# Kernel tuning notes

Measured on AMD Instinct MI355X. Metric: run time of the kernel, lower is better.

The kernel has to match this reference:

```python
import jax, jax.numpy as jnp
import numpy as np

D_MODEL = 1024
N_HEADS = 16
D_FF = 4 * D_MODEL
CTX = 2048
EPS = 1e-5


def setup_inputs() -> dict:
    key = jax.random.key(0)
    ks = jax.random.split(key, 8)
    s = 0.02
    z = jax.random.normal(ks[0], (2, CTX, D_MODEL), dtype=jnp.float32)
    W_Q = jax.random.normal(ks[1], (D_MODEL, D_MODEL), dtype=jnp.float32) * s
    W_K = jax.random.normal(ks[2], (D_MODEL, D_MODEL), dtype=jnp.float32) * s
    W_V = jax.random.normal(ks[3], (D_MODEL, D_MODEL), dtype=jnp.float32) * s
    W_O = jax.random.normal(ks[4], (D_MODEL, D_MODEL), dtype=jnp.float32) * s
    W_fc = jax.random.normal(ks[5], (D_MODEL, D_FF), dtype=jnp.float32) * s
    W_proj = jax.random.normal(ks[6], (D_FF, D_MODEL), dtype=jnp.float32) * s
    g1 = jnp.ones((D_MODEL,), dtype=jnp.float32)
    g2 = jnp.ones((D_MODEL,), dtype=jnp.float32)
    return {"z": z, "W_Q": W_Q, "W_K": W_K, "W_V": W_V, "W_O": W_O,
            "W_fc": W_fc, "W_proj": W_proj, "g1": g1, "g2": g2}


def rmsnorm(x, gain):
    rms = jnp.sqrt(jnp.sum(x * x, axis=-1, keepdims=True) / x.shape[-1] + EPS)
    return (x / rms) * gain


def gelu_erf(x):
    return x * 0.5 * (1.0 + jax.lax.erf(x / jnp.sqrt(2.0).astype(x.dtype)))


def attention(zn, W_Q, W_K, W_V, W_O):
    B, T, D = zn.shape
    H = N_HEADS
    dh = D // H
    # [B,T,D] -> [B,H,T,dh]
    def split(x):
        return x.reshape(B, T, H, dh).transpose(0, 2, 1, 3)
    Q = split(zn @ W_Q)
    K = split(zn @ W_K)
    V = split(zn @ W_V)
    scores = jnp.einsum('bhtd,bhsd->bhts', Q, K) / jnp.sqrt(jnp.float32(dh))
    causal = jnp.triu(jnp.ones((T, T), dtype=bool), k=1)  # True above diagonal -> masked
    scores = jnp.where(causal[None, None], -jnp.inf, scores)
    weights = jax.nn.softmax(scores, axis=-1)
    ctx = jnp.einsum('bhts,bhsd->bhtd', weights, V)
    ctx = ctx.transpose(0, 2, 1, 3).reshape(B, T, D)
    return ctx @ W_O


def reference(z, W_Q, W_K, W_V, W_O, W_fc, W_proj, g1, g2):
    # pre-norm GPT block: z + attn(norm1(z)); then + ffn(norm2(z))
    z = z + attention(rmsnorm(z, g1), W_Q, W_K, W_V, W_O)
    h = rmsnorm(z, g2)
    ffn = gelu_erf(h @ W_fc) @ W_proj
    return z + ffn
```

## Files before the change

### kernel.cpp

```cpp
#include <hip/hip_runtime.h>
#include <hip/hip_bf16.h>
#include <math.h>


typedef __bf16 bf16x8 __attribute__((ext_vector_type(8)));
typedef float  f32x4  __attribute__((ext_vector_type(4)));

#define MFMA_16x16x32_BF16(A, B, C) __builtin_amdgcn_mfma_f32_16x16x32_bf16((A), (B), (C), 0, 0, 0)

#define GLDS16(g, l) __builtin_amdgcn_global_load_lds( \
    (const __attribute__((address_space(1))) void*)(g), \
    (__attribute__((address_space(3))) void*)(l), 16, 0, 0)

__global__ __launch_bounds__(256) void transconv_all_kernel(
    const float* __restrict__ W_Q, const float* __restrict__ W_K,
    const float* __restrict__ W_V, const float* __restrict__ W_O,
    const float* __restrict__ W_fc, const float* __restrict__ W_proj,
    __bf16* __restrict__ WtQKV, __bf16* __restrict__ WtO,
    __bf16* __restrict__ Wtfc, __bf16* __restrict__ Wtproj)
{
    const int id = blockIdx.x;
    const float* src;
    __bf16* dst;
    int K, N, nx, t;
    if (id < 4096) {
        const int wsel = id >> 10;
        t = id & 1023;
        src = (wsel == 0) ? W_Q : (wsel == 1) ? W_K : (wsel == 2) ? W_V : W_O;
        dst = (wsel < 3) ? (WtQKV + (size_t)wsel * 1048576) : WtO;
        K = 1024; N = 1024; nx = 32;
    } else if (id < 8192) {
        t = id - 4096; src = W_fc; dst = Wtfc; K = 1024; N = 4096; nx = 128;
    } else {
        t = id - 8192; src = W_proj; dst = Wtproj; K = 4096; N = 1024; nx = 32;
    }
    const int n0 = (t % nx) * 32, k0 = (t / nx) * 32;

    __shared__ float tile[32][33];
    const int c = threadIdx.x & 31, r = threadIdx.x >> 5;
#pragma unroll
    for (int i = 0; i < 4; ++i)
        tile[r + 8 * i][c] = src[(size_t)(k0 + r + 8 * i) * N + n0 + c];
    __syncthreads();
#pragma unroll
    for (int i = 0; i < 4; ++i)
        dst[(size_t)(n0 + r + 8 * i) * K + k0 + c] = (__bf16)tile[c][r + 8 * i];
}

__global__ __launch_bounds__(256) void rmsnorm_kernel(
    const float* __restrict__ x, const float* __restrict__ gain,
    __bf16* __restrict__ out)
{
    const int row = blockIdx.x, t = threadIdx.x;
    const float4 v = ((const float4*)(x + (size_t)row * 1024))[t];
    float ss = v.x * v.x + v.y * v.y + v.z * v.z + v.w * v.w;
#pragma unroll
    for (int m = 1; m < 64; m <<= 1) ss += __shfl_xor(ss, m);
    __shared__ float red[4];
    const int wid = t >> 6, lane = t & 63;
    if (lane == 0) red[wid] = ss;
    __syncthreads();
    const float tot = red[0] + red[1] + red[2] + red[3];
    const float inv = rsqrtf(tot * (1.0f / 1024.0f) + 1e-5f);
    const float4 gv = ((const float4*)gain)[t];
    __bf16* o = out + (size_t)row * 1024 + t * 4;
    o[0] = (__bf16)(v.x * inv * gv.x);
    o[1] = (__bf16)(v.y * inv * gv.y);
    o[2] = (__bf16)(v.z * inv * gv.z);
    o[3] = (__bf16)(v.w * inv * gv.w);
}

template <int EPI>
__device__ __forceinline__ void epi_write(
    void* outp, const float* res, int N, int rowg, int colg, float v)
{
    if constexpr (EPI == 1) {
        const size_t idx = (size_t)rowg * N + colg;
        ((float*)outp)[idx] = res[idx] + v;
    } else if constexpr (EPI == 2) {
        const size_t idx = (size_t)rowg * N + colg;
        ((__bf16*)outp)[idx] =
            (__bf16)(0.5f * v * (1.0f + erff(v * 0.70710678118654752f)));
    } else if constexpr (EPI == 3) {
        const size_t idx = (size_t)rowg * N + colg;
        ((float*)outp)[idx] += v;
    } else {
        __bf16* base = (__bf16*)outp;
        const int seg = colg >> 10;
        const int cg = colg & 1023;
        if (seg < 2) {
            base[(size_t)seg * 4194304 + (size_t)rowg * 1024 + cg] = (__bf16)v;
        } else {
            const int tt = rowg & 2047;
            const int r32 = tt & 31;
            const int p = ((r32 & 12) << 1) | ((r32 >> 2) & 4) | (r32 & 3);
            base[8388608 +
                 ((size_t)((rowg >> 11) * 16 + (cg >> 6)) * 64 + (cg & 63)) * 2048 +
                 ((tt & ~31) | p)] = (__bf16)v;
        }
    }
}

template <int EPI>
__global__ __launch_bounds__(512, 2) void gemm256(
    const __bf16* __restrict__ A, const __bf16* __restrict__ Bt,
    void* __restrict__ outp, const float* __restrict__ res,
    int M, int N, int K)
{
    __shared__ __bf16 As[2][2][128 * 64];
    __shared__ __bf16 Bs[2][2][128 * 64];
    const int tid = threadIdx.x;

    const int gx = gridDim.x, nwg = gx * gridDim.y;
    int bid = blockIdx.y * gx + blockIdx.x;
    if ((nwg & 7) == 0) bid = (bid & 7) * (nwg >> 3) + (bid >> 3);
    const int m0 = (bid / gx) * 256, n0 = (bid % gx) * 256;

    const int lane = tid & 63, w = tid >> 6;
    const int wr = w >> 2, wc = w & 3;
    const int lr = lane & 15, g = lane >> 4;
    const int srow8 = lane >> 3, schunk = (lane & 7) ^ srow8;
    const int xk = lr & 7;
    const int wch = wc >> 1, bro = (wc & 1) * 64;

    const __bf16* Ab = A + (size_t)m0 * K;
    const __bf16* Bb = Bt + (size_t)n0 * K;

    auto STG = [&](const __bf16* gb, __bf16* lds, int kt, int half) {
        const __bf16* src = gb + (size_t)(half * 128) * K + (kt << 6);
#pragma unroll
        for (int j = 0; j < 2; ++j) {
            const int sidx = j * 8 + w;
            GLDS16(src + (size_t)(sidx * 8 + srow8) * K + schunk * 8, lds + sidx * 512);
        }
    };

    f32x4 acc[8][4] = {};
    bf16x8 af[2][4], bf[2][4];

#define LAF(BUF, QM) do {                                                       \
    _Pragma("unroll") for (int i_ = 0; i_ < 4; ++i_)                            \
    _Pragma("unroll") for (int kk_ = 0; kk_ < 2; ++kk_)                         \
        af[kk_][i_] = *(const bf16x8*)&As[BUF][wr]                              \
            [((QM) * 64 + i_ * 16 + lr) * 64 + (((kk_ * 4 + g) ^ xk) << 3)];    \
    } while (0)

#define LBF(BUF, QN) do {                                                       \
    _Pragma("unroll") for (int i_ = 0; i_ < 2; ++i_)                            \
    _Pragma("unroll") for (int kk_ = 0; kk_ < 2; ++kk_)                         \
        bf[kk_][(QN) * 2 + i_] = *(const bf16x8*)&Bs[BUF][wch]                  \
            [(bro + ((QN) * 2 + i_) * 16 + lr) * 64 + (((kk_ * 4 + g) ^ xk) << 3)]; \
    } while (0)

#define MMQ(QM, QN) do {                                                        \
    __builtin_amdgcn_s_setprio(1);                                              \
    _Pragma("unroll") for (int kk_ = 0; kk_ < 2; ++kk_)                         \
    _Pragma("unroll") for (int i_ = 0; i_ < 4; ++i_)                            \
    _Pragma("unroll") for (int n_ = 0; n_ < 2; ++n_)                            \
        acc[(QM) * 4 + i_][(QN) * 2 + n_] = MFMA_16x16x32_BF16(                 \
            af[kk_][i_], bf[kk_][(QN) * 2 + n_], acc[(QM) * 4 + i_][(QN) * 2 + n_]); \
    __builtin_amdgcn_s_setprio(0);                                              \
    } while (0)

#define BAR()  __builtin_amdgcn_s_barrier()
#define VMC(N_) asm volatile("s_waitcnt vmcnt(" #N_ ")" ::: "memory")
#define SGB0() __builtin_amdgcn_sched_barrier(0)

    const int nt = K >> 6, niter = nt >> 1;

    STG(Ab, &As[0][0][0], 0, 0); STG(Ab, &As[0][1][0], 0, 1);
    STG(Bb, &Bs[0][0][0], 0, 0); STG(Bb, &Bs[0][1][0], 0, 1);
    STG(Bb, &Bs[1][0][0], 1, 0); STG(Bb, &Bs[1][1][0], 1, 1);

    for (int i = 0; i < niter - 1; ++i) {
        const int t1 = 2 * i + 1;
        STG(Ab, &As[1][0][0], t1, 0);
        VMC(6); BAR(); SGB0();
        LAF(0, 0); LBF(0, 0); MMQ(0, 0); BAR();
        LBF(0, 1); STG(Ab, &As[1][1][0], t1, 1); BAR(); MMQ(0, 1); BAR();
        LAF(0, 1); STG(Bb, &Bs[0][0][0], t1 + 1, 0); BAR(); MMQ(1, 0); BAR();
        STG(Bb, &Bs[0][1][0], t1 + 1, 1); BAR(); MMQ(1, 1); BAR();
        STG(Ab, &As[0][0][0], t1 + 1, 0);
        VMC(6); BAR(); SGB0();
        LAF(1, 0); LBF(1, 0); MMQ(0, 0); BAR();
        LBF(1, 1); STG(Ab, &As[0][1][0], t1 + 1, 1); BAR(); MMQ(0, 1); BAR();
        LAF(1, 1); STG(Bb, &Bs[1][0][0], t1 + 2, 0); BAR(); MMQ(1, 0); BAR();
        STG(Bb, &Bs[1][1][0], t1 + 2, 1); BAR(); MMQ(1, 1); BAR();
    }
    {
        STG(Ab, &As[1][0][0], nt - 1, 0);
        VMC(6); BAR(); SGB0();
        LAF(0, 0); LBF(0, 0); MMQ(0, 0); BAR();
        LBF(0, 1); STG(Ab, &As[1][1][0], nt - 1, 1); BAR(); MMQ(0, 1); BAR();
        LAF(0, 1); BAR(); MMQ(1, 0); BAR();
        BAR(); MMQ(1, 1); BAR();
        VMC(0); BAR(); SGB0();
        LAF(1, 0); LBF(1, 0); MMQ(0, 0); BAR();
        LBF(1, 1); BAR(); MMQ(0, 1); BAR();
        LAF(1, 1); BAR(); MMQ(1, 0); BAR();
        BAR(); MMQ(1, 1); BAR();
    }
#undef LAF
#undef LBF
#undef MMQ
#undef BAR
#undef VMC
#undef SGB0

#pragma unroll
    for (int mi = 0; mi < 8; ++mi)
#pragma unroll
        for (int ni = 0; ni < 4; ++ni) {
            const int colg = n0 + wc * 64 + ni * 16 + lr;
#pragma unroll
            for (int r = 0; r < 4; ++r) {
                const int rowg = m0 + wr * 128 + mi * 16 + 4 * g + r;
                epi_write<EPI>(outp, res, N, rowg, colg, acc[mi][ni][r]);
            }
        }
}

template <int BM, int BN, int EPI>
__global__ __launch_bounds__(256) void gemm_bf16(
    const __bf16* __restrict__ A, const __bf16* __restrict__ Bt,
    void* __restrict__ outp, const float* __restrict__ res,
    int M, int N, int K)
{
    __shared__ __bf16 As[2][BM * 64];
    __shared__ __bf16 Bs[2][BN * 64];
    const int tid = threadIdx.x;

    const int gx = gridDim.x, nwg = gx * gridDim.y;
    int bid = blockIdx.y * gx + blockIdx.x;
    if ((nwg & 7) == 0) bid = (bid & 7) * (nwg >> 3) + (bid >> 3);
    const int m0 = (bid / gx) * BM, n0 = (bid % gx) * BN;

    const int lane = tid & 63, w = tid >> 6;
    const int wm = w >> 1, wn = w & 1;
    const int lr = lane & 15, g = lane >> 4;
    const int srow = lane >> 3;
    const int scol = ((lane & 7) ^ srow) * 8;
    const int xr8 = lr & 7;

    constexpr int MI = BM / 32, NI = BN / 32;
    f32x4 acc[MI][NI] = {};

    const __bf16* Abase = A + (size_t)m0 * K;
    const __bf16* Bbase = Bt + (size_t)n0 * K;

    auto STAGE = [&](int kb, int buf) {
#pragma unroll
        for (int j = 0; j < BM / 32; ++j) {
            const int s = j * 4 + w;
            GLDS16(Abase + (size_t)(s * 8 + srow) * K + kb + scol, &As[buf][s * 512]);
        }
#pragma unroll
        for (int j = 0; j < BN / 32; ++j) {
            const int s = j * 4 + w;
            GLDS16(Bbase + (size_t)(s * 8 + srow) * K + kb + scol, &Bs[buf][s * 512]);
        }
    };

    const int nt = K >> 6;
    STAGE(0, 0);
    __syncthreads();

    for (int t = 0; t < nt; ++t) {
        const int cur = t & 1;
        if (t + 1 < nt) STAGE((t + 1) << 6, cur ^ 1);

        bf16x8 af[2][MI], bfr[2][NI];
#pragma unroll
        for (int kk = 0; kk < 2; ++kk) {
#pragma unroll
            for (int i = 0; i < MI; ++i)
                af[kk][i] = *(const bf16x8*)
                    &As[cur][(wm * (BM / 2) + i * 16 + lr) * 64 + (((kk * 4 + g) ^ xr8) << 3)];
#pragma unroll
            for (int i = 0; i < NI; ++i)
                bfr[kk][i] = *(const bf16x8*)
                    &Bs[cur][(wn * (BN / 2) + i * 16 + lr) * 64 + (((kk * 4 + g) ^ xr8) << 3)];
        }
#pragma unroll
        for (int kk = 0; kk < 2; ++kk)
#pragma unroll
            for (int mi = 0; mi < MI; ++mi)
#pragma unroll
                for (int ni = 0; ni < NI; ++ni)
                    acc[mi][ni] = MFMA_16x16x32_BF16(af[kk][mi], bfr[kk][ni], acc[mi][ni]);
        if (t + 1 < nt) __syncthreads();
    }

#pragma unroll
    for (int mi = 0; mi < MI; ++mi)
#pragma unroll
        for (int ni = 0; ni < NI; ++ni) {
            const int colg = n0 + wn * (BN / 2) + ni * 16 + lr;
#pragma unroll
            for (int r = 0; r < 4; ++r) {
                const int rowg = m0 + wm * (BM / 2) + mi * 16 + 4 * g + r;
                epi_write<EPI>(outp, res, N, rowg, colg, acc[mi][ni][r]);
            }
        }
}

__global__ __launch_bounds__(256) void attn_kernel(
    const __bf16* __restrict__ Q, const __bf16* __restrict__ Kb,
    const __bf16* __restrict__ Vt, __bf16* __restrict__ ctx)
{
    const int Dm = 1024, T = 2048;
    const int tid = threadIdx.x;
    const int w = tid >> 6, lane = tid & 63;
    const int lr = lane & 15, g = lane >> 4;
    const int bx = blockIdx.x;
    const int j = bx >> 5, bh = bx & 31, b = bh >> 4, h = bh & 15;
    const int qc = (j < 8) ? j : (j < 16) ? 39 - j : (j < 24) ? j - 8 : 47 - j;
    const int qbase = qc * 64 + w * 16;
    const size_t rowoff = (size_t)b * T;
    const __bf16* Qp = Q + rowoff * Dm + h * 64;
    const __bf16* Kp = Kb + rowoff * Dm + h * 64;
    const __bf16* Vtp = Vt + (size_t)bh * 64 * 2048;

    __shared__ __bf16 Ks[2][64 * 64];
    __shared__ __bf16 Vs[2][64 * 64];

    bf16x8 qf0 = *(const bf16x8*)&Qp[(size_t)(qbase + lr) * Dm + g * 8];
    bf16x8 qf1 = *(const bf16x8*)&Qp[(size_t)(qbase + lr) * Dm + 32 + g * 8];
    const float qsc = 0.125f * 1.44269504088896340736f;
#pragma unroll
    for (int jj = 0; jj < 8; ++jj) {
        qf0[jj] = (__bf16)((float)qf0[jj] * qsc);
        qf1[jj] = (__bf16)((float)qf1[jj] * qsc);
    }

    const int srow = lane >> 3;
    const int schunk = (lane & 7) ^ srow;

    f32x4 acc[4] = {};
    float m_s = -__builtin_inff(), l_s = 0.0f;
    const int nsteps = qc + 1;
    const f32x4 zacc = {0.0f, 0.0f, 0.0f, 0.0f};
    const int xr = (lr & 7) << 3;
    const int qg = qbase + lr;

#pragma unroll
    for (int jj = 0; jj < 2; ++jj) {
        const int row = jj * 32 + w * 8 + srow;
        GLDS16(Kp + (size_t)row * Dm + schunk * 8, &Ks[0][(jj * 32 + w * 8) * 64]);
        GLDS16(Vtp + (size_t)row * T + schunk * 8, &Vs[0][(jj * 32 + w * 8) * 64]);
    }
    __syncthreads();

    for (int t = 0; t < nsteps; ++t) {
        const int kvb = t * 64, cur = t & 1;
        if (t + 1 < nsteps) {
#pragma unroll
            for (int jj = 0; jj < 2; ++jj) {
                const int row = jj * 32 + w * 8 + srow;
                GLDS16(Kp + (size_t)(kvb + 64 + row) * Dm + schunk * 8,
                       &Ks[cur ^ 1][(jj * 32 + w * 8) * 64]);
                GLDS16(Vtp + (size_t)row * T + kvb + 64 + schunk * 8,
                       &Vs[cur ^ 1][(jj * 32 + w * 8) * 64]);
            }
        }

        float sv[4][4];
#pragma unroll
        for (int s4 = 0; s4 < 4; ++s4) {
            const int kv0 = kvb + s4 * 16;
            if (kv0 <= qbase + 15) {
                const int row = s4 * 16 + lr;
                const bf16x8 kfa = *(const bf16x8*)&Ks[cur][row * 64 + ((g * 8) ^ xr)];
                const bf16x8 kfb = *(const bf16x8*)&Ks[cur][row * 64 + ((32 + g * 8) ^ xr)];
                f32x4 st = MFMA_16x16x32_BF16(kfa, qf0, zacc);
                st = MFMA_16x16x32_BF16(kfb, qf1, st);
                const bool domask = (kv0 + 15 > qbase);
#pragma unroll
                for (int r = 0; r < 4; ++r) {
                    float x = st[r];
                    if (domask && (kv0 + 4 * g + r > qg)) x = -__builtin_inff();
                    sv[s4][r] = x;
                }
            } else {
#pragma unroll
                for (int r = 0; r < 4; ++r) sv[s4][r] = -__builtin_inff();
            }
        }

        float tm = sv[0][0];
#pragma unroll
        for (int s4 = 0; s4 < 4; ++s4)
#pragma unroll
            for (int r = 0; r < 4; ++r) tm = fmaxf(tm, sv[s4][r]);
        tm = fmaxf(tm, __shfl_xor(tm, 16));
        tm = fmaxf(tm, __shfl_xor(tm, 32));

        float m_use = m_s;
        if (!__all(tm - m_s <= 11.5f)) {
            m_use = fmaxf(m_s, tm);
            const float corr = exp2f(m_s - m_use);
            l_s *= corr;
            float cr[4];
#pragma unroll
            for (int r = 0; r < 4; ++r) cr[r] = __shfl(corr, 4 * g + r);
#pragma unroll
            for (int ct = 0; ct < 4; ++ct) {
                acc[ct][0] *= cr[0]; acc[ct][1] *= cr[1];
                acc[ct][2] *= cr[2]; acc[ct][3] *= cr[3];
            }
            m_s = m_use;
        }

        float rs = 0.0f;
#pragma unroll
        for (int s4 = 0; s4 < 4; ++s4)
#pragma unroll
            for (int r = 0; r < 4; ++r) {
                sv[s4][r] = exp2f(sv[s4][r] - m_use);
                rs += sv[s4][r];
            }
        rs += __shfl_xor(rs, 16);
        rs += __shfl_xor(rs, 32);
        l_s += rs;

        bf16x8 pa0, pa1;
#pragma unroll
        for (int r = 0; r < 4; ++r) {
            pa0[r] = (__bf16)sv[0][r];
            pa0[4 + r] = (__bf16)sv[1][r];
            pa1[r] = (__bf16)sv[2][r];
            pa1[4 + r] = (__bf16)sv[3][r];
        }
        const bool liveB = (kvb + 32 <= qbase + 15);
#pragma unroll
        for (int ct = 0; ct < 4; ++ct) {
            const __bf16* vrow = &Vs[cur][(ct * 16 + lr) * 64];
            const bf16x8 vf = *(const bf16x8*)&vrow[(8 * g) ^ xr];
            acc[ct] = MFMA_16x16x32_BF16(pa0, vf, acc[ct]);
            if (liveB) {
                const bf16x8 vf2 = *(const bf16x8*)&vrow[(32 + 8 * g) ^ xr];
                acc[ct] = MFMA_16x16x32_BF16(pa1, vf2, acc[ct]);
            }
        }
        __syncthreads();
    }

    const float il = __builtin_amdgcn_rcpf(l_s);
    float dn[4];
#pragma unroll
    for (int r = 0; r < 4; ++r) dn[r] = __shfl(il, 4 * g + r);
#pragma unroll
    for (int ct = 0; ct < 4; ++ct)
#pragma unroll
        for (int r = 0; r < 4; ++r)
            ctx[(rowoff + qbase + 4 * g + r) * Dm + h * 64 + ct * 16 + lr] =
                (__bf16)(acc[ct][r] * dn[r]);
}

extern "C" void kernel_launch(void* const* d_in, const int* in_sizes, int n_in,
                              void* d_out, int out_size, void* d_ws, size_t ws_size,
                              hipStream_t stream)
{
    (void)in_sizes; (void)n_in; (void)out_size; (void)ws_size;
    const float* z      = (const float*)d_in[0];
    const float* W_Q    = (const float*)d_in[1];
    const float* W_K    = (const float*)d_in[2];
    const float* W_V    = (const float*)d_in[3];
    const float* W_O    = (const float*)d_in[4];
    const float* W_fc   = (const float*)d_in[5];
    const float* W_proj = (const float*)d_in[6];
    const float* g1     = (const float*)d_in[7];
    const float* g2     = (const float*)d_in[8];
    float* out = (float*)d_out;

    char* ws = (char*)d_ws;
    const size_t MB = (size_t)1 << 20;
    __bf16* WtQKV  = (__bf16*)(ws + 0 * MB);
    __bf16* WtO    = (__bf16*)(ws + 6 * MB);
    __bf16* Wtfc   = (__bf16*)(ws + 8 * MB);
    __bf16* Wtproj = (__bf16*)(ws + 16 * MB);
    __bf16* zn     = (__bf16*)(ws + 24 * MB);
    __bf16* Qb     = (__bf16*)(ws + 32 * MB);
    __bf16* Kbuf   = (__bf16*)(ws + 40 * MB);
    __bf16* Vtb    = (__bf16*)(ws + 48 * MB);
    __bf16* ffn1   = (__bf16*)(ws + 40 * MB);
    __bf16* ctx    = zn;
    __bf16* hb     = Qb;

    const int Tt = 2048, Dm = 1024, Bb = 2, M = Bb * Tt, DFF = 4096;
    const dim3 blk256(256), blk512(512);

    transconv_all_kernel<<<12288, blk256, 0, stream>>>(
        W_Q, W_K, W_V, W_O, W_fc, W_proj, WtQKV, WtO, Wtfc, Wtproj);

    rmsnorm_kernel<<<M, blk256, 0, stream>>>(z, g1, zn);

    gemm_bf16<128, 64, 4><<<dim3(48, 32), blk256, 0, stream>>>(
        zn, WtQKV, Qb, nullptr, M, 3072, Dm);

    attn_kernel<<<1024, blk256, 0, stream>>>(Qb, Kbuf, Vtb, ctx);

    gemm_bf16<128, 64, 1><<<dim3(16, 32), blk256, 0, stream>>>(
        ctx, WtO, out, z, M, Dm, Dm);

    rmsnorm_kernel<<<M, blk256, 0, stream>>>(out, g2, hb);

    gemm256<2><<<dim3(16, 16), blk512, 0, stream>>>(
        hb, Wtfc, ffn1, nullptr, M, DFF, Dm);

    gemm_bf16<128, 64, 3><<<dim3(16, 32), blk256, 0, stream>>>(
        ffn1, Wtproj, out, nullptr, M, Dm, DFF);
}
```

Measured before the change: 269.9 us.

## Split-K the FFN down-projection with a reduce kernel; enlarge QKV GEMM tile

The FFN projection GEMM (K=4096) now runs as a split-K launch over two halves with 128x128 tiles. Each half writes fp32 partials to workspace, and a separate reduce kernel adds both partials into the output. The QKV GEMM also moves to 128x128 tiles with half as many blocks. This is meant to improve per-block reuse and keep more blocks busy on the long-K GEMM, at the cost of extra partial-buffer traffic and one more kernel launch.

```diff
diff --git a/kernel.cpp b/kernel.cpp
--- a/kernel.cpp
+++ b/kernel.cpp
@@ -68,6 +68,20 @@
     o[1] = (__bf16)(v.y * inv * gv.y);
     o[2] = (__bf16)(v.z * inv * gv.z);
     o[3] = (__bf16)(v.w * inv * gv.w);
+}
+
+__global__ __launch_bounds__(256) void reduce_add_kernel(
+    float* __restrict__ out, const float* __restrict__ p0,
+    const float* __restrict__ p1, int n4)
+{
+    for (int i = blockIdx.x * 256 + threadIdx.x; i < n4; i += gridDim.x * 256) {
+        const float4 a = ((const float4*)p0)[i];
+        const float4 b = ((const float4*)p1)[i];
+        float4 o = ((float4*)out)[i];
+        o.x += a.x + b.x; o.y += a.y + b.y;
+        o.z += a.z + b.z; o.w += a.w + b.w;
+        ((float4*)out)[i] = o;
+    }
 }
 
 template <int EPI>
@@ -224,7 +238,7 @@
 __global__ __launch_bounds__(256) void gemm_bf16(
     const __bf16* __restrict__ A, const __bf16* __restrict__ Bt,
     void* __restrict__ outp, const float* __restrict__ res,
-    int M, int N, int K)
+    int M, int N, int K, int Kld)
 {
     __shared__ __bf16 As[2][BM * 64];
     __shared__ __bf16 Bs[2][BN * 64];
@@ -245,19 +259,19 @@
     constexpr int MI = BM / 32, NI = BN / 32;
     f32x4 acc[MI][NI] = {};
 
-    const __bf16* Abase = A + (size_t)m0 * K;
-    const __bf16* Bbase = Bt + (size_t)n0 * K;
+    const __bf16* Abase = A + (size_t)m0 * Kld + blockIdx.z * K;
+    const __bf16* Bbase = Bt + (size_t)n0 * Kld + blockIdx.z * K;
 
     auto STAGE = [&](int kb, int buf) {
 #pragma unroll
         for (int j = 0; j < BM / 32; ++j) {
             const int s = j * 4 + w;
-            GLDS16(Abase + (size_t)(s * 8 + srow) * K + kb + scol, &As[buf][s * 512]);
+            GLDS16(Abase + (size_t)(s * 8 + srow) * Kld + kb + scol, &As[buf][s * 512]);
         }
 #pragma unroll
         for (int j = 0; j < BN / 32; ++j) {
             const int s = j * 4 + w;
-            GLDS16(Bbase + (size_t)(s * 8 + srow) * K + kb + scol, &Bs[buf][s * 512]);
+            GLDS16(Bbase + (size_t)(s * 8 + srow) * Kld + kb + scol, &Bs[buf][s * 512]);
         }
     };
 
@@ -299,7 +313,13 @@
 #pragma unroll
             for (int r = 0; r < 4; ++r) {
                 const int rowg = m0 + wm * (BM / 2) + mi * 16 + 4 * g + r;
-                epi_write<EPI>(outp, res, N, rowg, colg, acc[mi][ni][r]);
+                const float v = acc[mi][ni][r];
+                if constexpr (EPI == 5) {
+                    float* pout = (blockIdx.z == 0) ? (float*)outp : (float*)(void*)res;
+                    pout[(size_t)rowg * N + colg] = v;
+                } else {
+                    epi_write<EPI>(outp, res, N, rowg, colg, v);
+                }
             }
         }
 }
@@ -484,6 +504,8 @@
     __bf16* Kbuf   = (__bf16*)(ws + 40 * MB);
     __bf16* Vtb    = (__bf16*)(ws + 48 * MB);
     __bf16* ffn1   = (__bf16*)(ws + 40 * MB);
+    float*  part0  = (float*)(ws + 0 * MB);
+    float*  part1  = (float*)(ws + 24 * MB);
     __bf16* ctx    = zn;
     __bf16* hb     = Qb;
 
@@ -495,19 +517,21 @@
 
     rmsnorm_kernel<<<M, blk256, 0, stream>>>(z, g1, zn);
 
-    gemm_bf16<128, 64, 4><<<dim3(48, 32), blk256, 0, stream>>>(
-        zn, WtQKV, Qb, nullptr, M, 3072, Dm);
+    gemm_bf16<128, 128, 4><<<dim3(24, 32), blk256, 0, stream>>>(
+        zn, WtQKV, Qb, nullptr, M, 3072, Dm, Dm);
 
     attn_kernel<<<1024, blk256, 0, stream>>>(Qb, Kbuf, Vtb, ctx);
 
     gemm_bf16<128, 64, 1><<<dim3(16, 32), blk256, 0, stream>>>(
-        ctx, WtO, out, z, M, Dm, Dm);
+        ctx, WtO, out, z, M, Dm, Dm, Dm);
 
     rmsnorm_kernel<<<M, blk256, 0, stream>>>(out, g2, hb);
 
     gemm256<2><<<dim3(16, 16), blk512, 0, stream>>>(
         hb, Wtfc, ffn1, nullptr, M, DFF, Dm);
 
-    gemm_bf16<128, 64, 3><<<dim3(16, 32), blk256, 0, stream>>>(
-        ffn1, Wtproj, out, nullptr, M, Dm, DFF);
-}
+    gemm_bf16<128, 128, 5><<<dim3(8, 32, 2), blk256, 0, stream>>>(
+        ffn1, Wtproj, part0, (const float*)part1, M, Dm, DFF / 2, DFF);
+
+    reduce_add_kernel<<<2048, blk256, 0, stream>>>(out, part0, part1, M * Dm / 4);
+}
```

After: 258.8 us. 4.1% less time.
